# Kernel optimization log

Hardware: AMD Instinct MI355X
Metric: run time of the kernel (lower is better)

The kernel has to match this reference:

```python
import jax, jax.numpy as jnp
import numpy as np

N_NODES = 100000


def high_pass_filter(z, src, dst, n):
    # add self loops (PyG add_self_loops appends [i, i] edges)
    loop = jnp.arange(n, dtype=src.dtype)
    src2 = jnp.concatenate([src, loop])
    dst2 = jnp.concatenate([dst, loop])
    ones = jnp.ones(src2.shape[0], dtype=z.dtype)
    # deg = degree(edge_index[0]) -> out-degree counts per source node
    deg = jax.ops.segment_sum(ones, src2, num_segments=n)
    # mean aggregation at target nodes: out[i] = mean_{(j->i)} z[j]
    msg_sum = jax.ops.segment_sum(z[src2], dst2, num_segments=n)
    cnt = jax.ops.segment_sum(ones, dst2, num_segments=n)
    mean_out = msg_sum / cnt[:, None]  # cnt >= 1 thanks to self loops
    return z - mean_out / deg[:, None]


def setup_inputs() -> dict:
    key = jax.random.key(0)
    k = jax.random.split(key, 8)
    d = 64
    E = 1200000
    x = jax.random.normal(k[0], (N_NODES, d), dtype=jnp.float32)
    edge_index = jax.random.randint(k[1], (2, E), 0, N_NODES, dtype=jnp.int64)
    s = 1.0 / np.sqrt(d)
    W1 = jax.random.uniform(k[2], (d, d), jnp.float32, -s, s)
    b1 = jax.random.uniform(k[3], (d,), jnp.float32, -s, s)
    W2 = jax.random.uniform(k[4], (d, d), jnp.float32, -s, s)
    b2 = jax.random.uniform(k[5], (d,), jnp.float32, -s, s)
    W3 = jax.random.uniform(k[6], (d, d), jnp.float32, -s, s)
    b3 = jax.random.uniform(k[7], (d,), jnp.float32, -s, s)
    return {"x": x, "edge_index": edge_index, "W1": W1, "b1": b1,
            "W2": W2, "b2": b2, "W3": W3, "b3": b3}


def reference(x, edge_index, W1, b1, W2, b2, W3, b3):
    src, dst = edge_index[0], edge_index[1]
    n = x.shape[0]
    z = jax.nn.relu(x @ W1 + b1)
    z = high_pass_filter(z, src, dst, n)
    z = jax.nn.relu(z @ W2 + b2)
    z = high_pass_filter(z, src, dst, n)
    z = jax.nn.relu(z @ W3 + b3)
    return z
```

## Files before the change

kernel.cpp:

```cpp
#include <hip/hip_runtime.h>

#define D 64
#define CAP 48
#define CAPB 3584
#define BIN_CHUNK 2048
#define LDS_STRIDE 68

typedef unsigned int uint;
typedef unsigned short ushort;

__device__ __forceinline__ ushort f2bf(float f) {
    uint u = __float_as_uint(f);
    return (ushort)((u + 0x7FFFu + ((u >> 16) & 1u)) >> 16);
}

#define SWZ(c, k4) ((((k4) ^ (((c) >> 2) & 7)) << 2))

__global__ void k_zero(int* __restrict__ p, int n) {
    int i = blockIdx.x * blockDim.x + threadIdx.x;
    if (i < n) p[i] = 0;
}

__global__ __launch_bounds__(256) void k_bin2(
    const int* __restrict__ src, const int* __restrict__ dst, int E, int nb,
    int* __restrict__ gcur, int* __restrict__ binD, int* __restrict__ binS)
{
    __shared__ int curD[512], curS[512];
    const int t = threadIdx.x;
    for (int i = t; i < nb; i += 256) { curD[i] = 0; curS[i] = 0; }
    __syncthreads();

    const int e0 = blockIdx.x * BIN_CHUNK;
    int sv[8], dv[8];
#pragma unroll
    for (int i = 0; i < 8; ++i) {
        int e = e0 + i * 256 + t;
        if (e < E) {
            sv[i] = src[e]; dv[i] = dst[e];
            atomicAdd(&curD[dv[i] >> 8], 1);
            atomicAdd(&curS[sv[i] >> 8], 1);
        } else {
            sv[i] = -1;
        }
    }
    __syncthreads();
    for (int i = t; i < nb; i += 256) {
        int c = curD[i]; curD[i] = c ? atomicAdd(&gcur[i], c) : 0;
        c = curS[i];     curS[i] = c ? atomicAdd(&gcur[nb + i], c) : 0;
    }
    __syncthreads();
#pragma unroll
    for (int i = 0; i < 8; ++i) {
        if (sv[i] >= 0) {
            int b = dv[i] >> 8;
            int pos = atomicAdd(&curD[b], 1);
            if (pos < CAPB) binD[(size_t)b * CAPB + pos] = ((dv[i] & 255) << 17) | sv[i];
            b = sv[i] >> 8;
            pos = atomicAdd(&curS[b], 1);
            if (pos < CAPB) binS[(size_t)b * CAPB + pos] = sv[i] & 255;
        }
    }
}

__device__ void gemm_body(const float* z, const float* __restrict__ W,
                          const float* __restrict__ bias, float* out,
                          ushort* zh_out, int n, float* sX, float* sWT, int tile)
{
    const int t = threadIdx.x;
    const int row0 = tile << 6;

    for (int i = 0; i < 4; ++i) {
        int s = i * 256 + t;
        int k = s >> 4;
        int c4 = (s & 15) << 2;
        float4 w = ((const float4*)W)[s];
        int kk = SWZ(c4 + 0, k >> 2) + (k & 3);
        sWT[(c4 + 0) * LDS_STRIDE + kk] = w.x;
        kk = SWZ(c4 + 1, k >> 2) + (k & 3);
        sWT[(c4 + 1) * LDS_STRIDE + kk] = w.y;
        kk = SWZ(c4 + 2, k >> 2) + (k & 3);
        sWT[(c4 + 2) * LDS_STRIDE + kk] = w.z;
        kk = SWZ(c4 + 3, k >> 2) + (k & 3);
        sWT[(c4 + 3) * LDS_STRIDE + kk] = w.w;
    }
    for (int i = 0; i < 4; ++i) {
        int s = i * 256 + t;
        int r = s >> 4;
        int grow = row0 + r;
        float4 v = make_float4(0.f, 0.f, 0.f, 0.f);
        if (grow < n) v = ((const float4*)(z + (size_t)grow * D))[s & 15];
        *((float4*)(sX + r * LDS_STRIDE + ((s & 15) << 2))) = v;
    }
    __syncthreads();

    const int tc = (t & 15) << 2;
    const int tr = (t >> 4) << 2;

    float acc[4][4] = {};
#define DOT4(a_, w_, acc_) \
    acc_ = fmaf((a_).x, (w_).x, fmaf((a_).y, (w_).y, fmaf((a_).z, (w_).z, fmaf((a_).w, (w_).w, acc_))))
    for (int k4 = 0; k4 < 16; ++k4) {
        float4 a0 = *(const float4*)(sX + (tr + 0) * LDS_STRIDE + (k4 << 2));
        float4 a1 = *(const float4*)(sX + (tr + 1) * LDS_STRIDE + (k4 << 2));
        float4 a2 = *(const float4*)(sX + (tr + 2) * LDS_STRIDE + (k4 << 2));
        float4 a3 = *(const float4*)(sX + (tr + 3) * LDS_STRIDE + (k4 << 2));
        float4 w0 = *(const float4*)(sWT + (tc + 0) * LDS_STRIDE + SWZ(tc + 0, k4));
        float4 w1 = *(const float4*)(sWT + (tc + 1) * LDS_STRIDE + SWZ(tc + 1, k4));
        float4 w2 = *(const float4*)(sWT + (tc + 2) * LDS_STRIDE + SWZ(tc + 2, k4));
        float4 w3 = *(const float4*)(sWT + (tc + 3) * LDS_STRIDE + SWZ(tc + 3, k4));
        DOT4(a0, w0, acc[0][0]); DOT4(a0, w1, acc[0][1]); DOT4(a0, w2, acc[0][2]); DOT4(a0, w3, acc[0][3]);
        DOT4(a1, w0, acc[1][0]); DOT4(a1, w1, acc[1][1]); DOT4(a1, w2, acc[1][2]); DOT4(a1, w3, acc[1][3]);
        DOT4(a2, w0, acc[2][0]); DOT4(a2, w1, acc[2][1]); DOT4(a2, w2, acc[2][2]); DOT4(a2, w3, acc[2][3]);
        DOT4(a3, w0, acc[3][0]); DOT4(a3, w1, acc[3][1]); DOT4(a3, w2, acc[3][2]); DOT4(a3, w3, acc[3][3]);
    }
#undef DOT4

    float b0 = bias[tc + 0], b1 = bias[tc + 1], b2 = bias[tc + 2], b3 = bias[tc + 3];
    for (int rr = 0; rr < 4; ++rr) {
        int grow = row0 + tr + rr;
        if (grow >= n) continue;
        float4 o;
        o.x = fmaxf(acc[rr][0] + b0, 0.f);
        o.y = fmaxf(acc[rr][1] + b1, 0.f);
        o.z = fmaxf(acc[rr][2] + b2, 0.f);
        o.w = fmaxf(acc[rr][3] + b3, 0.f);
        ((float4*)(out + (size_t)grow * D))[tc >> 2] = o;
        if (zh_out) {
            short4 h;
            h.x = (short)f2bf(o.x); h.y = (short)f2bf(o.y);
            h.z = (short)f2bf(o.z); h.w = (short)f2bf(o.w);
            *(short4*)(zh_out + (size_t)grow * D + tc) = h;
        }
    }
}

__global__ __launch_bounds__(256) void k_finishG(
    const int* __restrict__ gcur, const int* __restrict__ binD,
    const int* __restrict__ binS, int n, int nb,
    int* __restrict__ csr, int* __restrict__ icnt, float* __restrict__ inv,
    const float* __restrict__ x, const float* __restrict__ W1,
    const float* __restrict__ b1, float* __restrict__ zA,
    ushort* __restrict__ zh, int ntiles)
{
    __shared__ float smem[2 * 64 * LDS_STRIDE];
    if (blockIdx.x >= nb) {
        gemm_body(x, W1, b1, zA, zh, n, smem, smem + 64 * LDS_STRIDE,
                  blockIdx.x - nb);
        return;
    }
    int* cur = (int*)smem;
    int* od  = (int*)smem + 256;
    const int b = blockIdx.x, t = threadIdx.x;
    cur[t] = 0; od[t] = 0;
    __syncthreads();

    int cntD = gcur[b]; if (cntD > CAPB) cntD = CAPB;
    const int* bb = binD + (size_t)b * CAPB;
    for (int i = t; i < cntD; i += 256) {
        int v = bb[i];
        int dloc = v >> 17;
        int pos = atomicAdd(&cur[dloc], 1);
        if (pos < CAP) csr[(size_t)((b << 8) + dloc) * CAP + pos] = v & 0x1FFFF;
    }
    int cntS = gcur[nb + b]; if (cntS > CAPB) cntS = CAPB;
    const int* bs = binS + (size_t)b * CAPB;
    for (int i = t; i < cntS; i += 256) {
        atomicAdd(&od[bs[i]], 1);
    }
    __syncthreads();
    int node = (b << 8) + t;
    if (node < n) {
        int ic = cur[t]; if (ic > CAP) ic = CAP;
        icnt[node] = ic;
        inv[node] = 1.0f / ((float)(od[t] + 1) * (float)(ic + 1));
    }
}

__global__ __launch_bounds__(256) void k_gemm(
    const float* z, const float* __restrict__ W, const float* __restrict__ bias,
    float* out, ushort* zh_out, int n)
{
    __shared__ float smem[2 * 64 * LDS_STRIDE];
    gemm_body(z, W, bias, out, zh_out, n, smem, smem + 64 * LDS_STRIDE, blockIdx.x);
}

__global__ __launch_bounds__(256) void k_aggr(
    const float* __restrict__ zA, const ushort* __restrict__ zh,
    const int* __restrict__ icnt, const int* __restrict__ csr,
    const float* __restrict__ inv, int n, float* __restrict__ zB)
{
    int q = (blockIdx.x * 256 + threadIdx.x) >> 6;
    int lane = threadIdx.x & 63;
    int c8 = (lane & 7) << 3;
    int j = lane >> 3;
    int w0 = q << 1;
    int w1 = w0 + 1;
    if (w0 >= n) return;
    bool has1 = (w1 < n);

    int cnt0 = icnt[w0]; if (cnt0 > CAP) cnt0 = CAP;
    int cnt1 = has1 ? icnt[w1] : 0; if (cnt1 > CAP) cnt1 = CAP;
    int my0 = (lane < cnt0) ? csr[w0 * CAP + lane] : 0;
    int my1 = (lane < cnt1) ? csr[w1 * CAP + lane] : 0;
    int nit = ((cnt0 > cnt1 ? cnt0 : cnt1) + 7) >> 3;

    float a0[8] = {0.f, 0.f, 0.f, 0.f, 0.f, 0.f, 0.f, 0.f};
    float a1[8] = {0.f, 0.f, 0.f, 0.f, 0.f, 0.f, 0.f, 0.f};
    for (int it = 0; it < nit; ++it) {
        int e = (it << 3) + j;
        int s0 = __shfl(my0, e, 64);
        int s1 = __shfl(my1, e, 64);
        uint4 u0 = *(const uint4*)(zh + (size_t)s0 * D + c8);
        uint4 u1 = *(const uint4*)(zh + (size_t)s1 * D + c8);
        if (e < cnt0) {
            a0[0] += __uint_as_float(u0.x << 16);
            a0[1] += __uint_as_float(u0.x & 0xFFFF0000u);
            a0[2] += __uint_as_float(u0.y << 16);
            a0[3] += __uint_as_float(u0.y & 0xFFFF0000u);
            a0[4] += __uint_as_float(u0.z << 16);
            a0[5] += __uint_as_float(u0.z & 0xFFFF0000u);
            a0[6] += __uint_as_float(u0.w << 16);
            a0[7] += __uint_as_float(u0.w & 0xFFFF0000u);
        }
        if (e < cnt1) {
            a1[0] += __uint_as_float(u1.x << 16);
            a1[1] += __uint_as_float(u1.x & 0xFFFF0000u);
            a1[2] += __uint_as_float(u1.y << 16);
            a1[3] += __uint_as_float(u1.y & 0xFFFF0000u);
            a1[4] += __uint_as_float(u1.z << 16);
            a1[5] += __uint_as_float(u1.z & 0xFFFF0000u);
            a1[6] += __uint_as_float(u1.w << 16);
            a1[7] += __uint_as_float(u1.w & 0xFFFF0000u);
        }
    }

    float iv0 = 0.f, iv1 = 0.f;
    float4 p00, p01, p10, p11;
    if (j == 0) {
        iv0 = inv[w0];
        const float* zr0 = zA + (size_t)w0 * D + c8;
        p00 = *(const float4*)zr0;
        p01 = *(const float4*)(zr0 + 4);
        if (has1) {
            iv1 = inv[w1];
            const float* zr1 = zA + (size_t)w1 * D + c8;
            p10 = *(const float4*)zr1;
            p11 = *(const float4*)(zr1 + 4);
        }
    }

#pragma unroll
    for (int m = 8; m <= 32; m <<= 1) {
#pragma unroll
        for (int i = 0; i < 8; ++i) a0[i] += __shfl_xor(a0[i], m, 64);
#pragma unroll
        for (int i = 0; i < 8; ++i) a1[i] += __shfl_xor(a1[i], m, 64);
    }

    if (j == 0) {
        float4 o0, o1;
        o0.x = fmaf(-(a0[0] + p00.x), iv0, p00.x);
        o0.y = fmaf(-(a0[1] + p00.y), iv0, p00.y);
        o0.z = fmaf(-(a0[2] + p00.z), iv0, p00.z);
        o0.w = fmaf(-(a0[3] + p00.w), iv0, p00.w);
        o1.x = fmaf(-(a0[4] + p01.x), iv0, p01.x);
        o1.y = fmaf(-(a0[5] + p01.y), iv0, p01.y);
        o1.z = fmaf(-(a0[6] + p01.z), iv0, p01.z);
        o1.w = fmaf(-(a0[7] + p01.w), iv0, p01.w);
        float* zo0 = zB + (size_t)w0 * D + c8;
        *(float4*)zo0 = o0;
        *(float4*)(zo0 + 4) = o1;
        if (has1) {
            float4 q0, q1;
            q0.x = fmaf(-(a1[0] + p10.x), iv1, p10.x);
            q0.y = fmaf(-(a1[1] + p10.y), iv1, p10.y);
            q0.z = fmaf(-(a1[2] + p10.z), iv1, p10.z);
            q0.w = fmaf(-(a1[3] + p10.w), iv1, p10.w);
            q1.x = fmaf(-(a1[4] + p11.x), iv1, p11.x);
            q1.y = fmaf(-(a1[5] + p11.y), iv1, p11.y);
            q1.z = fmaf(-(a1[6] + p11.z), iv1, p11.z);
            q1.w = fmaf(-(a1[7] + p11.w), iv1, p11.w);
            float* zo1 = zB + (size_t)w1 * D + c8;
            *(float4*)zo1 = q0;
            *(float4*)(zo1 + 4) = q1;
        }
    }
}

extern "C" void kernel_launch(void* const* d_in, const int* in_sizes, int n_in,
                              void* d_out, int out_size, void* d_ws, size_t ws_size,
                              hipStream_t stream) {
    const float* x  = (const float*)d_in[0];
    const int*   ei = (const int*)d_in[1];
    const float* W1 = (const float*)d_in[2];
    const float* b1 = (const float*)d_in[3];
    const float* W2 = (const float*)d_in[4];
    const float* b2 = (const float*)d_in[5];
    const float* W3 = (const float*)d_in[6];
    const float* b3 = (const float*)d_in[7];

    const int n = in_sizes[0] / D;
    const int E = in_sizes[1] / 2;
    const int* src = ei;
    const int* dst = ei + E;

    const int nb = (n + 255) >> 8;

    float*  zA   = (float*)d_ws;
    ushort* zh   = (ushort*)(zA + (size_t)n * D);
    float*  inv  = (float*)(zh + (size_t)n * D);
    int*    icnt = (int*)(inv + n);
    int*    csr  = icnt + n;
    int*    gcur = csr + (size_t)n * CAP;
    int*    binD = gcur + 2 * nb;
    int*    binS = binD + (size_t)nb * CAPB;

    float* out = (float*)d_out;
    dim3 blk(256);

    const int bin_blocks = (E + BIN_CHUNK - 1) / BIN_CHUNK;
    const int ntiles = (n + 63) >> 6;

    k_zero<<<dim3((2 * nb + 255) / 256), blk, 0, stream>>>(gcur, 2 * nb);
    k_bin2<<<dim3(bin_blocks), blk, 0, stream>>>(src, dst, E, nb, gcur, binD, binS);
    k_finishG<<<dim3(nb + ntiles), blk, 0, stream>>>(
        gcur, binD, binS, n, nb, csr, icnt, inv, x, W1, b1, zA, zh, ntiles);

    dim3 gemm_grid(ntiles);
    dim3 aggr_grid((n + 7) / 8);

    k_aggr<<<aggr_grid, blk, 0, stream>>>(zA, zh, icnt, csr, inv, n, zA);
    k_gemm<<<gemm_grid, blk, 0, stream>>>(zA, W2, b2, zA, zh, n);
    k_aggr<<<aggr_grid, blk, 0, stream>>>(zA, zh, icnt, csr, inv, n, zA);
    k_gemm<<<gemm_grid, blk, 0, stream>>>(zA, W3, b3, out, nullptr, n);
}
```

Measured before the change: 259.5 us.

## Stage binned edges in LDS via local prefix sum before coalesced global writes

The binning kernel now computes a block-local exclusive scan of per-bin counts, scatters each edge into a bin-sorted LDS staging buffer, and then writes to the global bins in order. The aim is to turn random scattered global stores into mostly contiguous runs per bin, which improves coalescing. In exchange it adds two 512-entry scans with many barriers and 16KB more LDS per block, which can lower occupancy.

```diff
diff --git a/kernel.cpp b/kernel.cpp
--- a/kernel.cpp
+++ b/kernel.cpp
@@ -25,9 +25,10 @@
     const int* __restrict__ src, const int* __restrict__ dst, int E, int nb,
     int* __restrict__ gcur, int* __restrict__ binD, int* __restrict__ binS)
 {
-    __shared__ int curD[512], curS[512];
+    __shared__ int hD[512], hS[512], sc[512], cur2[512];
+    __shared__ int sdata[BIN_CHUNK], sdest[BIN_CHUNK];
     const int t = threadIdx.x;
-    for (int i = t; i < nb; i += 256) { curD[i] = 0; curS[i] = 0; }
+    hD[t] = 0; hD[t + 256] = 0; hS[t] = 0; hS[t + 256] = 0;
     __syncthreads();
 
     const int e0 = blockIdx.x * BIN_CHUNK;
@@ -37,28 +38,81 @@
         int e = e0 + i * 256 + t;
         if (e < E) {
             sv[i] = src[e]; dv[i] = dst[e];
-            atomicAdd(&curD[dv[i] >> 8], 1);
-            atomicAdd(&curS[sv[i] >> 8], 1);
+            atomicAdd(&hD[dv[i] >> 8], 1);
+            atomicAdd(&hS[sv[i] >> 8], 1);
         } else {
             sv[i] = -1;
         }
     }
     __syncthreads();
-    for (int i = t; i < nb; i += 256) {
-        int c = curD[i]; curD[i] = c ? atomicAdd(&gcur[i], c) : 0;
-        c = curS[i];     curS[i] = c ? atomicAdd(&gcur[nb + i], c) : 0;
+
+    int nvalid = E - e0; if (nvalid > BIN_CHUNK) nvalid = BIN_CHUNK;
+
+    sc[t] = hD[t]; sc[t + 256] = hD[t + 256];
+    __syncthreads();
+    for (int off = 1; off < 512; off <<= 1) {
+        int v0 = (t >= off) ? sc[t - off] : 0;
+        int v1 = ((t + 256) >= off) ? sc[t + 256 - off] : 0;
+        __syncthreads();
+        sc[t] += v0; sc[t + 256] += v1;
+        __syncthreads();
+    }
+    for (int k = t; k < 512; k += 256) {
+        int h = hD[k];
+        int lb = sc[k] - h;
+        cur2[k] = lb;
+        int go = (k < nb && h) ? atomicAdd(&gcur[k], h) : 0;
+        sc[k] = k * CAPB + go - lb;
     }
     __syncthreads();
 #pragma unroll
     for (int i = 0; i < 8; ++i) {
         if (sv[i] >= 0) {
             int b = dv[i] >> 8;
-            int pos = atomicAdd(&curD[b], 1);
-            if (pos < CAPB) binD[(size_t)b * CAPB + pos] = ((dv[i] & 255) << 17) | sv[i];
-            b = sv[i] >> 8;
-            pos = atomicAdd(&curS[b], 1);
-            if (pos < CAPB) binS[(size_t)b * CAPB + pos] = sv[i] & 255;
-        }
+            int pos = atomicAdd(&cur2[b], 1);
+            int dabs = sc[b] + pos;
+            sdata[pos] = ((dv[i] & 255) << 17) | sv[i];
+            sdest[pos] = (dabs - b * CAPB < CAPB) ? dabs : -1;
+        }
+    }
+    __syncthreads();
+    for (int i = t; i < nvalid; i += 256) {
+        int d2 = sdest[i];
+        if (d2 >= 0) binD[d2] = sdata[i];
+    }
+    __syncthreads();
+
+    sc[t] = hS[t]; sc[t + 256] = hS[t + 256];
+    __syncthreads();
+    for (int off = 1; off < 512; off <<= 1) {
+        int v0 = (t >= off) ? sc[t - off] : 0;
+        int v1 = ((t + 256) >= off) ? sc[t + 256 - off] : 0;
+        __syncthreads();
+        sc[t] += v0; sc[t + 256] += v1;
+        __syncthreads();
+    }
+    for (int k = t; k < 512; k += 256) {
+        int h = hS[k];
+        int lb = sc[k] - h;
+        cur2[k] = lb;
+        int go = (k < nb && h) ? atomicAdd(&gcur[nb + k], h) : 0;
+        sc[k] = k * CAPB + go - lb;
+    }
+    __syncthreads();
+#pragma unroll
+    for (int i = 0; i < 8; ++i) {
+        if (sv[i] >= 0) {
+            int b = sv[i] >> 8;
+            int pos = atomicAdd(&cur2[b], 1);
+            int dabs = sc[b] + pos;
+            sdata[pos] = sv[i] & 255;
+            sdest[pos] = (dabs - b * CAPB < CAPB) ? dabs : -1;
+        }
+    }
+    __syncthreads();
+    for (int i = t; i < nvalid; i += 256) {
+        int d2 = sdest[i];
+        if (d2 >= 0) binS[d2] = sdata[i];
     }
 }
 
```

Result: no change. 260.2 us (+0.3%).
